# Kernel optimization log

Hardware: AMD Instinct MI355X
Metric: run time of the kernel (lower is better)

The kernel has to match this reference:

```python
import jax, jax.numpy as jnp
import numpy as np

NUM_EXPERT = 8
IN_FEAT = 1024
OUT_FEAT = 1024
N_TOKENS = 8192


def setup_inputs() -> dict:
    key = jax.random.key(0)
    k_inp, k_gate, k_w = jax.random.split(key, 3)
    inp = jax.random.normal(k_inp, (N_TOKENS, IN_FEAT), dtype=jnp.float32)
    gate = jax.random.randint(k_gate, (N_TOKENS,), 0, NUM_EXPERT, dtype=jnp.int32)
    # FMoELinear weight: [num_expert, out_feat, in_feat], kaiming-uniform-like init
    bound = 1.0 / np.sqrt(IN_FEAT)
    weight = jax.random.uniform(
        k_w, (NUM_EXPERT, OUT_FEAT, IN_FEAT), dtype=jnp.float32,
        minval=-bound, maxval=bound)
    return {"inp": inp, "gate": gate, "weight": weight}


def reference(inp, gate, weight):
    # out[i] = weight[gate[i]] @ inp[i]  (top-1 MoE dispatch + grouped GEMM + combine)
    # Loop over the small fixed expert set via scan; each step does a masked
    # dense GEMM so only tokens routed to expert e contribute.
    n, _ = inp.shape
    num_expert, out_feat, _ = weight.shape

    def body(acc, ew):
        e, w_e = ew  # w_e: [out_feat, in_feat]
        mask = (gate == e).astype(inp.dtype)[:, None]  # [n, 1]
        acc = acc + (inp * mask) @ w_e.T               # [n, out_feat]
        return acc, None

    init = jnp.zeros((n, out_feat), dtype=inp.dtype)
    out, _ = jax.lax.scan(body, init, (jnp.arange(num_expert), weight))
    return out
```

## Files before the change

kernel.cpp:

```cpp
#include <hip/hip_runtime.h>
#include <hip/hip_bf16.h>

#define N_TOKENS 8192
#define IN_FEAT 1024
#define OUT_FEAT 1024
#define NUM_EXPERT 8

#define BM 128
#define BN 128
#define BK 32

typedef __bf16 bf16x8 __attribute__((ext_vector_type(8)));
typedef float f32x4 __attribute__((ext_vector_type(4)));

__device__ __forceinline__ bf16x8 cvt8(float4 lo, float4 hi) {
    bf16x8 r;
    r[0] = (__bf16)lo.x; r[1] = (__bf16)lo.y;
    r[2] = (__bf16)lo.z; r[3] = (__bf16)lo.w;
    r[4] = (__bf16)hi.x; r[5] = (__bf16)hi.y;
    r[6] = (__bf16)hi.z; r[7] = (__bf16)hi.w;
    return r;
}


#define HIST1(G) do { int g_ = (G); unsigned long long m_;                   \
    m_ = __ballot(g_ == 0); c0 += (int)__popcll(m_);                         \
    m_ = __ballot(g_ == 1); c1 += (int)__popcll(m_);                         \
    m_ = __ballot(g_ == 2); c2 += (int)__popcll(m_);                         \
    m_ = __ballot(g_ == 3); c3 += (int)__popcll(m_);                         \
    m_ = __ballot(g_ == 4); c4 += (int)__popcll(m_);                         \
    m_ = __ballot(g_ == 5); c5 += (int)__popcll(m_);                         \
    m_ = __ballot(g_ == 6); c6 += (int)__popcll(m_);                         \
    m_ = __ballot(g_ == 7); c7 += (int)__popcll(m_); } while (0)

#define SCAT1(G, TOK) do { int g_ = (G); int tok_ = (TOK);                   \
    unsigned long long m_;                                                   \
    m_ = __ballot(g_ == 0);                                                  \
    if (g_ == 0) perm[o0 + (int)__popcll(m_ & lt)] = tok_;                   \
    o0 += (int)__popcll(m_);                                                 \
    m_ = __ballot(g_ == 1);                                                  \
    if (g_ == 1) perm[o1 + (int)__popcll(m_ & lt)] = tok_;                   \
    o1 += (int)__popcll(m_);                                                 \
    m_ = __ballot(g_ == 2);                                                  \
    if (g_ == 2) perm[o2 + (int)__popcll(m_ & lt)] = tok_;                   \
    o2 += (int)__popcll(m_);                                                 \
    m_ = __ballot(g_ == 3);                                                  \
    if (g_ == 3) perm[o3 + (int)__popcll(m_ & lt)] = tok_;                   \
    o3 += (int)__popcll(m_);                                                 \
    m_ = __ballot(g_ == 4);                                                  \
    if (g_ == 4) perm[o4 + (int)__popcll(m_ & lt)] = tok_;                   \
    o4 += (int)__popcll(m_);                                                 \
    m_ = __ballot(g_ == 5);                                                  \
    if (g_ == 5) perm[o5 + (int)__popcll(m_ & lt)] = tok_;                   \
    o5 += (int)__popcll(m_);                                                 \
    m_ = __ballot(g_ == 6);                                                  \
    if (g_ == 6) perm[o6 + (int)__popcll(m_ & lt)] = tok_;                   \
    o6 += (int)__popcll(m_);                                                 \
    m_ = __ballot(g_ == 7);                                                  \
    if (g_ == 7) perm[o7 + (int)__popcll(m_ & lt)] = tok_;                   \
    o7 += (int)__popcll(m_); } while (0)

__global__ __launch_bounds__(256) void moe_sort(const int* __restrict__ gate,
                                                int* __restrict__ perm,
                                                int* __restrict__ seg) {
    __shared__ int whist[4][NUM_EXPERT];
    __shared__ int wbase[4][NUM_EXPERT];
    const int t = threadIdx.x;
    const int wave = t >> 6, lane = t & 63;
    const unsigned long long lt = (lane == 0) ? 0ull : (~0ull >> (64 - lane));

    int c0 = 0, c1 = 0, c2 = 0, c3 = 0, c4 = 0, c5 = 0, c6 = 0, c7 = 0;
    #pragma unroll
    for (int j = 0; j < 8; ++j) {
        int4 vv = ((const int4*)gate)[j * 256 + t];
        HIST1(vv.x); HIST1(vv.y); HIST1(vv.z); HIST1(vv.w);
    }
    if (lane == 0) {
        whist[wave][0] = c0; whist[wave][1] = c1;
        whist[wave][2] = c2; whist[wave][3] = c3;
        whist[wave][4] = c4; whist[wave][5] = c5;
        whist[wave][6] = c6; whist[wave][7] = c7;
    }
    __syncthreads();

    if (t == 0) {
        int s = 0;
        #pragma unroll
        for (int e = 0; e < NUM_EXPERT; ++e) {
            seg[e] = s;
            int b = s;
            #pragma unroll
            for (int w = 0; w < 4; ++w) { wbase[w][e] = b; b += whist[w][e]; }
            s = b;
        }
        seg[NUM_EXPERT] = s;
    }
    __syncthreads();

    int o0 = wbase[wave][0], o1 = wbase[wave][1];
    int o2 = wbase[wave][2], o3 = wbase[wave][3];
    int o4 = wbase[wave][4], o5 = wbase[wave][5];
    int o6 = wbase[wave][6], o7 = wbase[wave][7];
    #pragma unroll
    for (int j = 0; j < 8; ++j) {
        int4 vv = ((const int4*)gate)[j * 256 + t];
        const int tb = j * 1024 + t * 4;
        SCAT1(vv.x, tb);
        SCAT1(vv.y, tb + 1);
        SCAT1(vv.z, tb + 2);
        SCAT1(vv.w, tb + 3);
    }
}

__global__ __launch_bounds__(256, 2) void moe_gemm_f(
    const float* __restrict__ inp,
    const float* __restrict__ weight,
    const int* __restrict__ perm,
    const int* __restrict__ seg,
    float* __restrict__ out) {

    const int bid = blockIdx.x;
    const int e = bid & 7;
    const int ntile = (bid >> 3) & 7;
    const int mtile = bid >> 6;

    const int base = seg[e];
    const int cnt = seg[e + 1] - base;
    if (mtile * BM >= cnt) return;
    const int tbase = base + mtile * BM;
    int rows = cnt - mtile * BM; if (rows > BM) rows = BM;

    __shared__ __align__(16) unsigned short lA[2][BM * BK];
    __shared__ __align__(16) unsigned short lB[2][BN * BK];

    const int t = threadIdx.x;

    const int crow = t >> 2;
    const int p = (t & 3) ^ (crow & 3);
    int ar0 = tbase + crow;       if (ar0 > N_TOKENS - 1) ar0 = N_TOKENS - 1;
    int ar1 = tbase + 64 + crow;  if (ar1 > N_TOKENS - 1) ar1 = N_TOKENS - 1;
    const float* gA0 = inp + (size_t)perm[ar0] * IN_FEAT + p * 8;
    const float* gA1 = inp + (size_t)perm[ar1] * IN_FEAT + p * 8;
    const float* gB0 = weight + (size_t)e * (OUT_FEAT * IN_FEAT)
                       + (ntile * BN + crow) * IN_FEAT + p * 8;
    const float* gB1 = gB0 + 64 * IN_FEAT;
    const int dofs = t * 8;
    const int dofs2 = (t + 256) * 8;

    const int wave = t >> 6;
    const int lane = t & 63;
    const int wm = (wave & 1) << 6;
    const int wn = (wave >> 1) << 6;
    const int l15 = lane & 15;
    const int quad = lane >> 4;
    const int qx = quad ^ (l15 & 3);
    const int fofsA = (wm + l15) * BK + qx * 8;
    const int fofsB = (wn + l15) * BK + qx * 8;

    f32x4 acc[4][4];
    #pragma unroll
    for (int i = 0; i < 4; ++i)
        #pragma unroll
        for (int j = 0; j < 4; ++j)
            acc[i][j] = (f32x4)0.0f;

    float4 ra0, ra1, ra2, ra3, rb0, rb1, rb2, rb3;

    ra0 = *(const float4*)(gA0);     ra1 = *(const float4*)(gA0 + 4);
    ra2 = *(const float4*)(gA1);     ra3 = *(const float4*)(gA1 + 4);
    rb0 = *(const float4*)(gB0);     rb1 = *(const float4*)(gB0 + 4);
    rb2 = *(const float4*)(gB1);     rb3 = *(const float4*)(gB1 + 4);
    *(bf16x8*)&lA[0][dofs]  = cvt8(ra0, ra1);
    *(bf16x8*)&lA[0][dofs2] = cvt8(ra2, ra3);
    *(bf16x8*)&lB[0][dofs]  = cvt8(rb0, rb1);
    *(bf16x8*)&lB[0][dofs2] = cvt8(rb2, rb3);

    #pragma unroll 1
    for (int s = 0; s < 32; ++s) {
        const int cur = s & 1;
        const int k0 = (s + 1) * BK;

        if (s < 31) {
            ra0 = *(const float4*)(gA0 + k0);     ra1 = *(const float4*)(gA0 + k0 + 4);
            ra2 = *(const float4*)(gA1 + k0);     ra3 = *(const float4*)(gA1 + k0 + 4);
            rb0 = *(const float4*)(gB0 + k0);     rb1 = *(const float4*)(gB0 + k0 + 4);
            rb2 = *(const float4*)(gB1 + k0);     rb3 = *(const float4*)(gB1 + k0 + 4);
        }

        __syncthreads();

        {
            bf16x8 af[4], bq[4];
            #pragma unroll
            for (int i = 0; i < 4; ++i)
                af[i] = *(const bf16x8*)&lA[cur][fofsA + i * 16 * BK];
            #pragma unroll
            for (int j = 0; j < 4; ++j)
                bq[j] = *(const bf16x8*)&lB[cur][fofsB + j * 16 * BK];
            #pragma unroll
            for (int i = 0; i < 4; ++i)
                #pragma unroll
                for (int j = 0; j < 4; ++j)
                    acc[i][j] = __builtin_amdgcn_mfma_f32_16x16x32_bf16(
                        af[i], bq[j], acc[i][j], 0, 0, 0);
        }

        if (s < 31) {
            *(bf16x8*)&lA[cur ^ 1][dofs]  = cvt8(ra0, ra1);
            *(bf16x8*)&lA[cur ^ 1][dofs2] = cvt8(ra2, ra3);
            *(bf16x8*)&lB[cur ^ 1][dofs]  = cvt8(rb0, rb1);
            *(bf16x8*)&lB[cur ^ 1][dofs2] = cvt8(rb2, rb3);
        }
    }

    #pragma unroll
    for (int mi = 0; mi < 4; ++mi) {
        #pragma unroll
        for (int r = 0; r < 4; ++r) {
            int row = wm + mi * 16 + quad * 4 + r;
            if (row < rows) {
                int token = perm[tbase + row];
                float* op = out + token * OUT_FEAT + ntile * BN + wn;
                #pragma unroll
                for (int ni = 0; ni < 4; ++ni)
                    op[ni * 16 + l15] = acc[mi][ni][r];
            }
        }
    }
}

extern "C" void kernel_launch(void* const* d_in, const int* in_sizes, int n_in,
                              void* d_out, int out_size, void* d_ws, size_t ws_size,
                              hipStream_t stream) {
    const float* inp = (const float*)d_in[0];
    const int* gate = (const int*)d_in[1];
    const float* weight = (const float*)d_in[2];
    float* out = (float*)d_out;

    int* perm = (int*)d_ws;
    int* seg = perm + N_TOKENS;

    moe_sort<<<1, 256, 0, stream>>>(gate, perm, seg);
    moe_gemm_f<<<4096, 256, 0, stream>>>(inp, weight, perm, seg, out);
}
```

Before: 147.9 us.

## Pre-convert inputs and weights to bf16, then async-load tiles into LDS

Adds a prep kernel that converts the fp32 activations and weights to bf16 in workspace, with the routing sort folded into block 0 of the same launch. A new GEMM kernel then streams the bf16 tiles straight into LDS with global_load_lds and processes two K-halves per double-buffer stage. This removes the per-tile fp32 loads and in-register conversion inside the GEMM and halves the bytes read there. The cost is an extra pass that reads all fp32 data and writes bf16 copies, and the path only runs when the workspace is large enough, falling back to the old kernels otherwise.

```diff
diff --git a/kernel.cpp b/kernel.cpp
--- a/kernel.cpp
+++ b/kernel.cpp
@@ -12,6 +12,17 @@
 
 typedef __bf16 bf16x8 __attribute__((ext_vector_type(8)));
 typedef float f32x4 __attribute__((ext_vector_type(4)));
+
+__device__ __forceinline__ unsigned int rne16(float x) {
+    union { float f; unsigned int u; } c;
+    c.f = x;
+    unsigned int u = c.u;
+    u += 0x7fffu + ((u >> 16) & 1u);
+    return u >> 16;
+}
+__device__ __forceinline__ unsigned int pk2(float x, float y) {
+    return rne16(x) | (rne16(y) << 16);
+}
 
 __device__ __forceinline__ bf16x8 cvt8(float4 lo, float4 hi) {
     bf16x8 r;
@@ -20,6 +31,13 @@
     r[4] = (__bf16)hi.x; r[5] = (__bf16)hi.y;
     r[6] = (__bf16)hi.z; r[7] = (__bf16)hi.w;
     return r;
+}
+
+__device__ __forceinline__ void load_lds16(const void* g, void* l) {
+    __builtin_amdgcn_global_load_lds(
+        (const __attribute__((address_space(1))) unsigned int*)g,
+        (__attribute__((address_space(3))) unsigned int*)l,
+        16, 0, 0);
 }
 
 
@@ -60,11 +78,10 @@
     if (g_ == 7) perm[o7 + (int)__popcll(m_ & lt)] = tok_;                   \
     o7 += (int)__popcll(m_); } while (0)
 
-__global__ __launch_bounds__(256) void moe_sort(const int* __restrict__ gate,
-                                                int* __restrict__ perm,
-                                                int* __restrict__ seg) {
-    __shared__ int whist[4][NUM_EXPERT];
-    __shared__ int wbase[4][NUM_EXPERT];
+__device__ __forceinline__ void sort_core(const int* __restrict__ gate,
+                                          int* __restrict__ perm,
+                                          int* __restrict__ seg,
+                                          int* whist, int* wbase) {
     const int t = threadIdx.x;
     const int wave = t >> 6, lane = t & 63;
     const unsigned long long lt = (lane == 0) ? 0ull : (~0ull >> (64 - lane));
@@ -76,10 +93,10 @@
         HIST1(vv.x); HIST1(vv.y); HIST1(vv.z); HIST1(vv.w);
     }
     if (lane == 0) {
-        whist[wave][0] = c0; whist[wave][1] = c1;
-        whist[wave][2] = c2; whist[wave][3] = c3;
-        whist[wave][4] = c4; whist[wave][5] = c5;
-        whist[wave][6] = c6; whist[wave][7] = c7;
+        whist[wave * 8 + 0] = c0; whist[wave * 8 + 1] = c1;
+        whist[wave * 8 + 2] = c2; whist[wave * 8 + 3] = c3;
+        whist[wave * 8 + 4] = c4; whist[wave * 8 + 5] = c5;
+        whist[wave * 8 + 6] = c6; whist[wave * 8 + 7] = c7;
     }
     __syncthreads();
 
@@ -90,17 +107,17 @@
             seg[e] = s;
             int b = s;
             #pragma unroll
-            for (int w = 0; w < 4; ++w) { wbase[w][e] = b; b += whist[w][e]; }
+            for (int w = 0; w < 4; ++w) { wbase[w * 8 + e] = b; b += whist[w * 8 + e]; }
             s = b;
         }
         seg[NUM_EXPERT] = s;
     }
     __syncthreads();
 
-    int o0 = wbase[wave][0], o1 = wbase[wave][1];
-    int o2 = wbase[wave][2], o3 = wbase[wave][3];
-    int o4 = wbase[wave][4], o5 = wbase[wave][5];
-    int o6 = wbase[wave][6], o7 = wbase[wave][7];
+    int o0 = wbase[wave * 8 + 0], o1 = wbase[wave * 8 + 1];
+    int o2 = wbase[wave * 8 + 2], o3 = wbase[wave * 8 + 3];
+    int o4 = wbase[wave * 8 + 4], o5 = wbase[wave * 8 + 5];
+    int o6 = wbase[wave * 8 + 6], o7 = wbase[wave * 8 + 7];
     #pragma unroll
     for (int j = 0; j < 8; ++j) {
         int4 vv = ((const int4*)gate)[j * 256 + t];
@@ -112,6 +129,163 @@
     }
 }
 
+__global__ __launch_bounds__(256) void moe_sort(const int* __restrict__ gate,
+                                                int* __restrict__ perm,
+                                                int* __restrict__ seg) {
+    __shared__ int whist[4 * NUM_EXPERT];
+    __shared__ int wbase[4 * NUM_EXPERT];
+    sort_core(gate, perm, seg, whist, wbase);
+}
+
+__global__ __launch_bounds__(256) void moe_prep_sort(
+    const float* __restrict__ inp,
+    const float* __restrict__ weight,
+    const int* __restrict__ gate,
+    int* __restrict__ perm,
+    int* __restrict__ seg,
+    unsigned int* __restrict__ A2,
+    unsigned int* __restrict__ W2) {
+
+    const int bid = blockIdx.x;
+    if (bid == 0) {
+        __shared__ int whist[4 * NUM_EXPERT];
+        __shared__ int wbase[4 * NUM_EXPERT];
+        sort_core(gate, perm, seg, whist, wbase);
+        return;
+    }
+    const int cid = bid - 1;
+    const int t = threadIdx.x;
+    const int wave = t >> 6, lane = t & 63;
+    const float* src;
+    unsigned int* dst;
+    if (cid < 2048) {
+        int row = cid * 4 + wave;
+        src = inp + row * IN_FEAT;
+        dst = A2 + row * (IN_FEAT / 2);
+    } else {
+        int row = (cid - 2048) * 4 + wave;
+        src = weight + row * IN_FEAT;
+        dst = W2 + row * (IN_FEAT / 2);
+    }
+    #pragma unroll
+    for (int j = 0; j < 4; ++j) {
+        float4 v = *(const float4*)(src + j * 256 + lane * 4);
+        uint2 o;
+        o.x = pk2(v.x, v.y);
+        o.y = pk2(v.z, v.w);
+        *(uint2*)(dst + j * 128 + lane * 2) = o;
+    }
+}
+
+__global__ __launch_bounds__(256, 2) void moe_gemm(
+    const unsigned short* __restrict__ A2,
+    const unsigned short* __restrict__ W2,
+    const int* __restrict__ perm,
+    const int* __restrict__ seg,
+    float* __restrict__ out) {
+
+    const int bid = blockIdx.x;
+    const int e = bid & 7;
+    const int ntile = (bid >> 3) & 7;
+    const int mtile = bid >> 6;
+
+    const int base = seg[e];
+    const int cnt = seg[e + 1] - base;
+    if (mtile * BM >= cnt) return;
+    const int tbase = base + mtile * BM;
+    int rows = cnt - mtile * BM; if (rows > BM) rows = BM;
+
+    __shared__ __align__(16) unsigned short lA[2][2][BM * BK];
+    __shared__ __align__(16) unsigned short lB[2][2][BN * BK];
+
+    const int t = threadIdx.x;
+
+    const int crow = t >> 2;
+    const int p = (t & 3) ^ (crow & 3);
+    int ar0 = tbase + crow;       if (ar0 > N_TOKENS - 1) ar0 = N_TOKENS - 1;
+    int ar1 = tbase + 64 + crow;  if (ar1 > N_TOKENS - 1) ar1 = N_TOKENS - 1;
+    const unsigned short* gA0 = A2 + (size_t)perm[ar0] * IN_FEAT + p * 8;
+    const unsigned short* gA1 = A2 + (size_t)perm[ar1] * IN_FEAT + p * 8;
+    const unsigned short* gB0 = W2 + (size_t)e * (OUT_FEAT * IN_FEAT)
+                                + (ntile * BN + crow) * IN_FEAT + p * 8;
+    const unsigned short* gB1 = gB0 + 64 * IN_FEAT;
+    const int dofs = t * 8;
+    const int dofs2 = (t + 256) * 8;
+
+    const int wave = t >> 6;
+    const int lane = t & 63;
+    const int wm = (wave & 1) << 6;
+    const int wn = (wave >> 1) << 6;
+    const int l15 = lane & 15;
+    const int quad = lane >> 4;
+    const int qx = quad ^ (l15 & 3);
+    const int fofsA = (wm + l15) * BK + qx * 8;
+    const int fofsB = (wn + l15) * BK + qx * 8;
+
+    f32x4 acc[4][4];
+    #pragma unroll
+    for (int i = 0; i < 4; ++i)
+        #pragma unroll
+        for (int j = 0; j < 4; ++j)
+            acc[i][j] = (f32x4)0.0f;
+
+    #define STAGE(s, buf, half) do {                                         \
+        load_lds16(gA0 + (s) * 32, &lA[buf][half][dofs]);                    \
+        load_lds16(gA1 + (s) * 32, &lA[buf][half][dofs2]);                   \
+        load_lds16(gB0 + (s) * 32, &lB[buf][half][dofs]);                    \
+        load_lds16(gB1 + (s) * 32, &lB[buf][half][dofs2]);                   \
+    } while (0)
+
+    #define COMPUTE(buf, half) do {                                          \
+        bf16x8 af[4], bq[4];                                                 \
+        _Pragma("unroll")                                                    \
+        for (int i = 0; i < 4; ++i)                                          \
+            af[i] = *(const bf16x8*)&lA[buf][half][fofsA + i * 16 * BK];     \
+        _Pragma("unroll")                                                    \
+        for (int j = 0; j < 4; ++j)                                          \
+            bq[j] = *(const bf16x8*)&lB[buf][half][fofsB + j * 16 * BK];     \
+        _Pragma("unroll")                                                    \
+        for (int i = 0; i < 4; ++i)                                          \
+            _Pragma("unroll")                                                \
+            for (int j = 0; j < 4; ++j)                                      \
+                acc[i][j] = __builtin_amdgcn_mfma_f32_16x16x32_bf16(         \
+                    af[i], bq[j], acc[i][j], 0, 0, 0);                       \
+    } while (0)
+
+    STAGE(0, 0, 0);
+    STAGE(1, 0, 1);
+
+    #pragma unroll 1
+    for (int i = 0; i < 16; ++i) {
+        const int b = i & 1;
+        __syncthreads();
+        if (i < 15) {
+            if (b == 0) { STAGE(2 * i + 2, 1, 0); STAGE(2 * i + 3, 1, 1); }
+            else        { STAGE(2 * i + 2, 0, 0); STAGE(2 * i + 3, 0, 1); }
+        }
+        if (b == 0) { COMPUTE(0, 0); COMPUTE(0, 1); }
+        else        { COMPUTE(1, 0); COMPUTE(1, 1); }
+    }
+
+    #undef STAGE
+    #undef COMPUTE
+
+    #pragma unroll
+    for (int mi = 0; mi < 4; ++mi) {
+        #pragma unroll
+        for (int r = 0; r < 4; ++r) {
+            int row = wm + mi * 16 + quad * 4 + r;
+            if (row < rows) {
+                int token = perm[tbase + row];
+                float* op = out + token * OUT_FEAT + ntile * BN + wn;
+                #pragma unroll
+                for (int ni = 0; ni < 4; ++ni)
+                    op[ni * 16 + l15] = acc[mi][ni][r];
+            }
+        }
+    }
+}
+
 __global__ __launch_bounds__(256, 2) void moe_gemm_f(
     const float* __restrict__ inp,
     const float* __restrict__ weight,
@@ -134,7 +308,6 @@
     __shared__ __align__(16) unsigned short lB[2][BN * BK];
 
     const int t = threadIdx.x;
-
     const int crow = t >> 2;
     const int p = (t & 3) ^ (crow & 3);
     int ar0 = tbase + crow;       if (ar0 > N_TOKENS - 1) ar0 = N_TOKENS - 1;
@@ -240,6 +413,17 @@
     int* perm = (int*)d_ws;
     int* seg = perm + N_TOKENS;
 
-    moe_sort<<<1, 256, 0, stream>>>(gate, perm, seg);
-    moe_gemm_f<<<4096, 256, 0, stream>>>(inp, weight, perm, seg, out);
-}
+    const size_t need = 65536 + 2ull * N_TOKENS * IN_FEAT * 2;
+    if (ws_size >= need) {
+        unsigned int* A2 = (unsigned int*)((char*)d_ws + 65536);
+        unsigned int* W2 = A2 + (N_TOKENS * IN_FEAT / 2);
+        moe_prep_sort<<<4097, 256, 0, stream>>>(inp, weight, gate, perm, seg,
+                                                A2, W2);
+        moe_gemm<<<4096, 256, 0, stream>>>((const unsigned short*)A2,
+                                           (const unsigned short*)W2,
+                                           perm, seg, out);
+    } else {
+        moe_sort<<<1, 256, 0, stream>>>(gate, perm, seg);
+        moe_gemm_f<<<4096, 256, 0, stream>>>(inp, weight, perm, seg, out);
+    }
+}
```

Result: slower. 152.0 us (+2.8%).
